# Optimization experiments

Measured on AMD Instinct MI355X. Metric: run time of the kernel, lower is better.

## Reference

```python
import jax, jax.numpy as jnp
import numpy as np

N = 100000
E = 1600000
DIMS = [128, 128, 64]


def _gcn_norm(edge_index, num_nodes):
    # PyG gcn_norm: add self-loops, symmetric normalization D^-1/2 (A+I) D^-1/2
    src, dst = edge_index[0], edge_index[1]
    loop = jnp.arange(num_nodes, dtype=src.dtype)
    src = jnp.concatenate([src, loop])
    dst = jnp.concatenate([dst, loop])
    deg = jax.ops.segment_sum(jnp.ones_like(src, dtype=jnp.float32), dst,
                              num_segments=num_nodes)
    dinv = jnp.where(deg > 0, jax.lax.rsqrt(deg), 0.0)
    w = dinv[src] * dinv[dst]  # [E+N]
    return src, dst, w


def _gcn_conv(x, src, dst, w, W, b):
    # transform first (cheaper when out_dim <= in_dim), then aggregate
    h = x @ W                                   # [N, out]
    msg = h[src] * w[:, None]                   # gather + scale  [E+N, out]
    out = jax.ops.segment_sum(msg, dst, num_segments=x.shape[0])
    return out + b


def setup_inputs() -> dict:
    key = jax.random.key(0)
    ks = jax.random.split(key, 6)
    x = jax.random.normal(ks[0], (N, DIMS[0]), dtype=jnp.float32)
    edge_index = jax.random.randint(ks[1], (2, E), 0, N, dtype=jnp.int64)
    # Glorot-style init for GCNConv weights, zero bias (PyG default)
    W1 = jax.random.normal(ks[2], (DIMS[0], DIMS[1]), dtype=jnp.float32) / np.sqrt(DIMS[0])
    b1 = jnp.zeros((DIMS[1],), dtype=jnp.float32)
    W2 = jax.random.normal(ks[3], (DIMS[1], DIMS[2]), dtype=jnp.float32) / np.sqrt(DIMS[1])
    b2 = jnp.zeros((DIMS[2],), dtype=jnp.float32)
    return {"x": x, "edge_index": edge_index, "W1": W1, "b1": b1, "W2": W2, "b2": b2}


def reference(x, edge_index, W1, b1, W2, b2):
    src, dst, w = _gcn_norm(edge_index, x.shape[0])
    h = _gcn_conv(x, src, dst, w, W1, b1)
    h = jax.nn.relu(h)
    # dropout is identity in eval mode (deterministic reference)
    out = _gcn_conv(h, src, dst, w, W2, b2)
    return out
```

## Files before the change

kernel.cpp:

```cpp
#include <hip/hip_runtime.h>
#include <hip/hip_fp16.h>

#define TPB 256
#define CHUNK 1024
#define EPB 4096
#define CSHIFT 8
#define AGG_BLOCKS 2048

typedef _Float16 half8 __attribute__((ext_vector_type(8)));
typedef float    f32x4 __attribute__((ext_vector_type(4)));


__global__ __launch_bounds__(256) void scanA_kernel(const int* __restrict__ cnt,
                                                    int* __restrict__ row_ptr,
                                                    int* __restrict__ chunk_sums, int n) {
    __shared__ int ls[256];
    const int t    = threadIdx.x;
    const int base = blockIdx.x * CHUNK;
    const int idx  = base + t * 4;
    int4 v = make_int4(0, 0, 0, 0);
    if (idx + 3 < n) v = *(const int4*)(cnt + idx);
    else {
        if (idx + 0 < n) v.x = cnt[idx + 0];
        if (idx + 1 < n) v.y = cnt[idx + 1];
        if (idx + 2 < n) v.z = cnt[idx + 2];
        if (idx + 3 < n) v.w = cnt[idx + 3];
    }
    int s0 = v.x, s1 = s0 + v.y, s2 = s1 + v.z, s3 = s2 + v.w;
    ls[t] = s3;
    __syncthreads();
    for (int off = 1; off < 256; off <<= 1) {
        int xv = (t >= off) ? ls[t - off] : 0;
        __syncthreads();
        ls[t] += xv;
        __syncthreads();
    }
    int excl = (t == 0) ? 0 : ls[t - 1];
    if (idx + 0 < n) row_ptr[idx + 0] = excl;
    if (idx + 1 < n) row_ptr[idx + 1] = excl + s0;
    if (idx + 2 < n) row_ptr[idx + 2] = excl + s1;
    if (idx + 3 < n) row_ptr[idx + 3] = excl + s2;
    if (t == 255) chunk_sums[blockIdx.x] = ls[255];
}

__global__ __launch_bounds__(256) void scanB_kernel(int* __restrict__ chunk_sums, int nch) {
    __shared__ int ls[256];
    const int t = threadIdx.x;
    ls[t] = (t < nch) ? chunk_sums[t] : 0;
    __syncthreads();
    for (int off = 1; off < 256; off <<= 1) {
        int xv = (t >= off) ? ls[t - off] : 0;
        __syncthreads();
        ls[t] += xv;
        __syncthreads();
    }
    if (t < nch) chunk_sums[t] = (t == 0) ? 0 : ls[t - 1];
}

__global__ __launch_bounds__(256) void scanC_kernel(int* __restrict__ row_ptr,
                                                    const int* __restrict__ chunk_sums, int n) {
    const int base = blockIdx.x * CHUNK;
    const int off  = chunk_sums[blockIdx.x];
    for (int k = threadIdx.x; k < CHUNK; k += 256) {
        int i = base + k;
        if (i < n) row_ptr[i] += off;
    }
}


__global__ __launch_bounds__(256) void hist_kernel(const int* __restrict__ dst,
                                                   int* __restrict__ hist_g,
                                                   int e, int nbc, int nblk) {
    __shared__ int hs[512];
    const int t = threadIdx.x;
    for (int i = t; i < nbc; i += 256) hs[i] = 0;
    __syncthreads();
    const int e0  = blockIdx.x * EPB;
    const int lim = min(e0 + EPB, e);
    for (int i = e0 + t; i < lim; i += 256)
        atomicAdd(&hs[dst[i] >> CSHIFT], 1);
    __syncthreads();
    for (int b = t; b < nbc; b += 256)
        hist_g[b * nblk + blockIdx.x] = hs[b];
}

__global__ __launch_bounds__(256) void partition_kernel(const int* __restrict__ src,
                                                        const int* __restrict__ dst,
                                                        const int* __restrict__ hist_scan,
                                                        int* __restrict__ pairs,
                                                        int e, int nbc, int nblk) {
    __shared__ int  hs[512];
    __shared__ int  lscan[512];
    __shared__ int  lfill[512];
    __shared__ int  base_s[512];
    __shared__ int  ls[256];
    __shared__ int2 sp[EPB];
    const int t = threadIdx.x;
    for (int i = t; i < nbc; i += 256) { hs[i] = 0; lfill[i] = 0; }
    __syncthreads();
    const int e0  = blockIdx.x * EPB;
    const int lim = min(e0 + EPB, e);
    for (int i = e0 + t; i < lim; i += 256)
        atomicAdd(&hs[dst[i] >> CSHIFT], 1);
    __syncthreads();
    int v0 = (2 * t     < nbc) ? hs[2 * t]     : 0;
    int v1 = (2 * t + 1 < nbc) ? hs[2 * t + 1] : 0;
    ls[t] = v0 + v1;
    __syncthreads();
    for (int off = 1; off < 256; off <<= 1) {
        int xv = (t >= off) ? ls[t - off] : 0;
        __syncthreads();
        ls[t] += xv;
        __syncthreads();
    }
    int excl = (t == 0) ? 0 : ls[t - 1];
    if (2 * t     < nbc) lscan[2 * t]     = excl;
    if (2 * t + 1 < nbc) lscan[2 * t + 1] = excl + v0;
    for (int b = t; b < nbc; b += 256) base_s[b] = hist_scan[b * nblk + blockIdx.x];
    __syncthreads();
    for (int i = e0 + t; i < lim; i += 256) {
        int d = dst[i];
        int b = d >> CSHIFT;
        int r = atomicAdd(&lfill[b], 1);
        sp[lscan[b] + r] = make_int2(src[i], d);
    }
    __syncthreads();
    const int cnt = lim - e0;
    for (int i = t; i < cnt; i += 256) {
        int2 pr = sp[i];
        int  b  = pr.y >> CSHIFT;
        pairs[base_s[b] + (i - lscan[b])] = pr.x | ((pr.y & 255) << 17);
    }
}

__global__ __launch_bounds__(256) void bucket_finalize_kernel(const int* __restrict__ pairs,
                                                              const int* __restrict__ hist_scan,
                                                              int* __restrict__ row_ptr,
                                                              float* __restrict__ dinv,
                                                              int* __restrict__ csr_src,
                                                              int n, int e, int nbc, int nblk) {
    __shared__ int cnt_s[256];
    __shared__ int fill[256];
    __shared__ int ls[256];
    const int b   = blockIdx.x;
    const int nb0 = b << CSHIFT;
    const int t   = threadIdx.x;
    const int r0  = hist_scan[b * nblk];
    const int r1  = (b + 1 < nbc) ? hist_scan[(b + 1) * nblk] : e;
    cnt_s[t] = 0;
    __syncthreads();
    for (int i = r0 + t; i < r1; i += 256)
        atomicAdd(&cnt_s[pairs[i] >> 17], 1);
    __syncthreads();
    int c = cnt_s[t];
    ls[t] = c;
    __syncthreads();
    for (int off = 1; off < 256; off <<= 1) {
        int xv = (t >= off) ? ls[t - off] : 0;
        __syncthreads();
        ls[t] += xv;
        __syncthreads();
    }
    int excl = (t == 0) ? 0 : ls[t - 1];
    int node = nb0 + t;
    if (node < n) {
        row_ptr[node] = r0 + excl;
        dinv[node]    = rsqrtf((float)(c + 1));
    }
    fill[t] = r0 + excl;
    __syncthreads();
    for (int i = r0 + t; i < r1; i += 256) {
        int pr = pairs[i];
        int p  = atomicAdd(&fill[pr >> 17], 1);
        csr_src[p] = pr & 0x1FFFF;
    }
    if (b == 0 && t == 0) row_ptr[n] = e;
}


template <int M, bool RELU, typename XT>
__global__ __launch_bounds__(256) void gemm_mfma_kernel(const XT* __restrict__ X,
                                                        const float* __restrict__ W,
                                                        const float* __restrict__ dinv,
                                                        __half* __restrict__ H, int nrows) {
    constexpr int NC = M / 16;
    __shared__ __align__(16) _Float16 Wf[NC * 4 * 64 * 8];

    const int tid = threadIdx.x;

    for (int f = tid; f < NC * 4 * 64; f += 256) {
        int c    = f >> 8;
        int i    = (f >> 6) & 3;
        int lane = f & 63;
        int quad = lane >> 4, n = lane & 15;
        const float* wp = W + (size_t)(i * 32 + quad * 8) * M + c * 16 + n;
        half8 hv;
#pragma unroll
        for (int j = 0; j < 8; ++j) hv[j] = (_Float16)wp[(size_t)j * M];
        ((half8*)Wf)[f] = hv;
    }
    __syncthreads();

    const int  wave = tid >> 6, lane = tid & 63;
    const int  quad = lane >> 4, n16 = lane & 15;
    const long rowbase = (long)blockIdx.x * 64 + wave * 16;

    long arow = rowbase + n16;
    const XT* xrow = X + (size_t)(arow < nrows ? arow : 0) * 128;
    half8 a[4];
    if constexpr (sizeof(XT) == 4) {
        const float4* xr = (const float4*)xrow;
#pragma unroll
        for (int i = 0; i < 4; ++i) {
            float4 x0 = xr[i * 8 + quad * 2];
            float4 x1 = xr[i * 8 + quad * 2 + 1];
            if (RELU) {
                x0.x = fmaxf(x0.x, 0.f); x0.y = fmaxf(x0.y, 0.f);
                x0.z = fmaxf(x0.z, 0.f); x0.w = fmaxf(x0.w, 0.f);
                x1.x = fmaxf(x1.x, 0.f); x1.y = fmaxf(x1.y, 0.f);
                x1.z = fmaxf(x1.z, 0.f); x1.w = fmaxf(x1.w, 0.f);
            }
            half8 hv;
            hv[0] = (_Float16)x0.x; hv[1] = (_Float16)x0.y;
            hv[2] = (_Float16)x0.z; hv[3] = (_Float16)x0.w;
            hv[4] = (_Float16)x1.x; hv[5] = (_Float16)x1.y;
            hv[6] = (_Float16)x1.z; hv[7] = (_Float16)x1.w;
            a[i] = hv;
        }
    } else {
        const half8* xr = (const half8*)xrow;
#pragma unroll
        for (int i = 0; i < 4; ++i) {
            half8 hv = xr[i * 4 + quad];
            if (RELU) {
#pragma unroll
                for (int j = 0; j < 8; ++j)
                    hv[j] = (hv[j] > (_Float16)0) ? hv[j] : (_Float16)0;
            }
            a[i] = hv;
        }
    }

    float dv[4];
#pragma unroll
    for (int r = 0; r < 4; ++r) {
        long orow = rowbase + quad * 4 + r;
        dv[r] = (orow < nrows) ? dinv[orow] : 0.f;
    }

    for (int c = 0; c < NC; ++c) {
        f32x4 acc = {0.f, 0.f, 0.f, 0.f};
#pragma unroll
        for (int i = 0; i < 4; ++i) {
            half8 b = ((const half8*)Wf)[(c * 4 + i) * 64 + lane];
            acc = __builtin_amdgcn_mfma_f32_16x16x32_f16(a[i], b, acc, 0, 0, 0);
        }
#pragma unroll
        for (int r = 0; r < 4; ++r) {
            long orow = rowbase + quad * 4 + r;
            if (orow < nrows)
                H[orow * M + c * 16 + n16] = __float2half(acc[r] * dv[r]);
        }
    }
}


__device__ __forceinline__ void add_u4(float2* a, const uint4& u) {
    float2 v0 = __half22float2(*(const __half2*)&u.x);
    float2 v1 = __half22float2(*(const __half2*)&u.y);
    float2 v2 = __half22float2(*(const __half2*)&u.z);
    float2 v3 = __half22float2(*(const __half2*)&u.w);
    a[0].x += v0.x; a[0].y += v0.y;
    a[1].x += v1.x; a[1].y += v1.y;
    a[2].x += v2.x; a[2].y += v2.y;
    a[3].x += v3.x; a[3].y += v3.y;
}


__global__ __launch_bounds__(TPB) void agg_pull128_kernel(const __half* __restrict__ hs,
                                                          const int* __restrict__ csr_src,
                                                          const int* __restrict__ row_ptr,
                                                          const float* __restrict__ dinv,
                                                          const float* __restrict__ bias,
                                                          __half* __restrict__ out, int n) {
    const int wid  = blockIdx.x * (TPB / 64) + (threadIdx.x >> 6);
    const int NW   = gridDim.x * (TPB / 64);
    const int lane = threadIdx.x & 63;
    const int q    = lane >> 4;
    const int sl   = lane & 15;
    if (wid >= n) return;
    const uint4* up   = (const uint4*)hs;
    const uint4* upsl = up + sl;

    const float4* bp = (const float4*)bias;
    const float4 bb0 = bp[2 * sl], bb1 = bp[2 * sl + 1];

    int b0 = row_ptr[wid], e0 = row_ptr[wid + 1];
    int nA = wid + NW;
    int b1 = 0, e1 = 0;
    if (nA < n) { b1 = row_ptr[nA]; e1 = row_ptr[nA + 1]; }
    int m0 = e0 - b0; if (m0 > 64) m0 = 64;
    int idx0 = (lane < m0) ? csr_src[b0 + lane] : 0;
    uint4 self0 = make_uint4(0, 0, 0, 0);
    if (q == 0) self0 = up[(size_t)wid * 16 + sl];
    float dv0 = dinv[wid];

    for (int ni = wid; ni < n; ni += NW) {
        const int n1 = ni + NW, n2 = ni + 2 * NW;
        int b2 = 0, e2 = 0;
        if (n2 < n) { b2 = row_ptr[n2]; e2 = row_ptr[n2 + 1]; }
        int idx1 = 0; uint4 self1 = make_uint4(0, 0, 0, 0); float dv1 = 0.f;
        if (n1 < n) {
            int m1 = e1 - b1; if (m1 > 64) m1 = 64;
            idx1 = (lane < m1) ? csr_src[b1 + lane] : 0;
            if (q == 0) self1 = up[(size_t)n1 * 16 + sl];
            dv1 = dinv[n1];
        }
        const int deg = e0 - b0;
        int m = deg; if (m > 64) m = 64;
        int sA0 = __shfl(idx0, q);
        int sA1 = __shfl(idx0, 4 + q);
        int sA2 = __shfl(idx0, 8 + q);
        int sA3 = __shfl(idx0, 12 + q);
        int sB0 = __shfl(idx0, 16 + q);
        int sB1 = __shfl(idx0, 20 + q);
        int sB2 = __shfl(idx0, 24 + q);
        int sB3 = __shfl(idx0, 28 + q);
        uint4 uA0 = upsl[(size_t)(unsigned)sA0 * 16];
        uint4 uA1 = upsl[(size_t)(unsigned)sA1 * 16];
        uint4 uA2 = upsl[(size_t)(unsigned)sA2 * 16];
        uint4 uA3 = upsl[(size_t)(unsigned)sA3 * 16];
        uint4 uB0 = upsl[(size_t)(unsigned)sB0 * 16];
        uint4 uB1 = upsl[(size_t)(unsigned)sB1 * 16];
        uint4 uB2 = upsl[(size_t)(unsigned)sB2 * 16];
        uint4 uB3 = upsl[(size_t)(unsigned)sB3 * 16];
        float2 a0[4], a1[4];
#pragma unroll
        for (int k = 0; k < 4; ++k) { a0[k] = make_float2(0.f, 0.f); a1[k] = make_float2(0.f, 0.f); }
        if (m >= 32) {
            add_u4(a0, uA0); add_u4(a1, uA1); add_u4(a0, uA2); add_u4(a1, uA3);
            add_u4(a0, uB0); add_u4(a1, uB1); add_u4(a0, uB2); add_u4(a1, uB3);
        } else {
            if (q < m)      add_u4(a0, uA0);
            if (4 + q < m)  add_u4(a1, uA1);
            if (8 + q < m)  add_u4(a0, uA2);
            if (12 + q < m) add_u4(a1, uA3);
            if (16 + q < m) add_u4(a0, uB0);
            if (20 + q < m) add_u4(a1, uB1);
            if (24 + q < m) add_u4(a0, uB2);
            if (28 + q < m) add_u4(a1, uB3);
        }
        for (int j = 32; j < m; j += 16) {
            int s0 = __shfl(idx0, j + q);
            int s1 = __shfl(idx0, j + 4 + q);
            int s2 = __shfl(idx0, j + 8 + q);
            int s3 = __shfl(idx0, j + 12 + q);
            uint4 u0 = upsl[(size_t)(unsigned)s0 * 16];
            uint4 u1 = upsl[(size_t)(unsigned)s1 * 16];
            uint4 u2 = upsl[(size_t)(unsigned)s2 * 16];
            uint4 u3 = upsl[(size_t)(unsigned)s3 * 16];
            if (j + q < m)      add_u4(a0, u0);
            if (j + 4 + q < m)  add_u4(a1, u1);
            if (j + 8 + q < m)  add_u4(a0, u2);
            if (j + 12 + q < m) add_u4(a1, u3);
        }
        for (int base = b0 + 64; base < e0; base += 64) {
            int mm = e0 - base; if (mm > 64) mm = 64;
            int idxv = (lane < mm) ? csr_src[base + lane] : 0;
            for (int j = 0; j < mm; j += 16) {
                int s0 = __shfl(idxv, j + q);
                int s1 = __shfl(idxv, j + 4 + q);
                int s2 = __shfl(idxv, j + 8 + q);
                int s3 = __shfl(idxv, j + 12 + q);
                uint4 u0 = upsl[(size_t)(unsigned)s0 * 16];
                uint4 u1 = upsl[(size_t)(unsigned)s1 * 16];
                uint4 u2 = upsl[(size_t)(unsigned)s2 * 16];
                uint4 u3 = upsl[(size_t)(unsigned)s3 * 16];
                if (j + q < mm)      add_u4(a0, u0);
                if (j + 4 + q < mm)  add_u4(a1, u1);
                if (j + 8 + q < mm)  add_u4(a0, u2);
                if (j + 12 + q < mm) add_u4(a1, u3);
            }
        }
#pragma unroll
        for (int k = 0; k < 4; ++k) { a0[k].x += a1[k].x; a0[k].y += a1[k].y; }
#pragma unroll
        for (int k = 0; k < 4; ++k) {
            a0[k].x += __shfl(a0[k].x, lane ^ 16);
            a0[k].y += __shfl(a0[k].y, lane ^ 16);
            a0[k].x += __shfl(a0[k].x, lane ^ 32);
            a0[k].y += __shfl(a0[k].y, lane ^ 32);
        }
        if (q == 0) {
            float2 v0 = __half22float2(*(const __half2*)&self0.x);
            float2 v1 = __half22float2(*(const __half2*)&self0.y);
            float2 v2 = __half22float2(*(const __half2*)&self0.z);
            float2 v3 = __half22float2(*(const __half2*)&self0.w);
            __half2 h0 = __floats2half2_rn(bb0.x + dv0 * (a0[0].x + v0.x),
                                           bb0.y + dv0 * (a0[0].y + v0.y));
            __half2 h1 = __floats2half2_rn(bb0.z + dv0 * (a0[1].x + v1.x),
                                           bb0.w + dv0 * (a0[1].y + v1.y));
            __half2 h2 = __floats2half2_rn(bb1.x + dv0 * (a0[2].x + v2.x),
                                           bb1.y + dv0 * (a0[2].y + v2.y));
            __half2 h3 = __floats2half2_rn(bb1.z + dv0 * (a0[3].x + v3.x),
                                           bb1.w + dv0 * (a0[3].y + v3.y));
            uint4 ov;
            ov.x = *(const unsigned*)&h0; ov.y = *(const unsigned*)&h1;
            ov.z = *(const unsigned*)&h2; ov.w = *(const unsigned*)&h3;
            ((uint4*)out)[(size_t)ni * 16 + sl] = ov;
        }
        b0 = b1; e0 = e1; idx0 = idx1; self0 = self1; dv0 = dv1;
        b1 = b2; e1 = e2;
    }
}


__global__ __launch_bounds__(TPB) void agg_pull64_kernel(const __half* __restrict__ hs,
                                                         const int* __restrict__ csr_src,
                                                         const int* __restrict__ row_ptr,
                                                         const float* __restrict__ dinv,
                                                         const float* __restrict__ bias,
                                                         float* __restrict__ out, int n) {
    const int wid  = blockIdx.x * (TPB / 64) + (threadIdx.x >> 6);
    const int NW   = gridDim.x * (TPB / 64);
    const int lane = threadIdx.x & 63;
    const int q    = lane >> 3;
    const int sl   = lane & 7;
    if (wid >= n) return;
    const uint4* up   = (const uint4*)hs;
    const uint4* upsl = up + sl;

    const float4* bp = (const float4*)bias;
    const float4 bb0 = bp[2 * sl], bb1 = bp[2 * sl + 1];

    int b0 = row_ptr[wid], e0 = row_ptr[wid + 1];
    int nA = wid + NW;
    int b1 = 0, e1 = 0;
    if (nA < n) { b1 = row_ptr[nA]; e1 = row_ptr[nA + 1]; }
    int m0 = e0 - b0; if (m0 > 64) m0 = 64;
    int idx0 = (lane < m0) ? csr_src[b0 + lane] : 0;
    uint4 self0 = make_uint4(0, 0, 0, 0);
    if (q == 0) self0 = up[(size_t)wid * 8 + sl];
    float dv0 = dinv[wid];

    for (int ni = wid; ni < n; ni += NW) {
        const int n1 = ni + NW, n2 = ni + 2 * NW;
        int b2 = 0, e2 = 0;
        if (n2 < n) { b2 = row_ptr[n2]; e2 = row_ptr[n2 + 1]; }
        int idx1 = 0; uint4 self1 = make_uint4(0, 0, 0, 0); float dv1 = 0.f;
        if (n1 < n) {
            int m1 = e1 - b1; if (m1 > 64) m1 = 64;
            idx1 = (lane < m1) ? csr_src[b1 + lane] : 0;
            if (q == 0) self1 = up[(size_t)n1 * 8 + sl];
            dv1 = dinv[n1];
        }
        const int deg = e0 - b0;
        int m = deg; if (m > 64) m = 64;
        int sA0 = __shfl(idx0, q);
        int sA1 = __shfl(idx0, 8 + q);
        int sB0 = __shfl(idx0, 16 + q);
        int sB1 = __shfl(idx0, 24 + q);
        uint4 uA0 = upsl[(size_t)(unsigned)sA0 * 8];
        uint4 uA1 = upsl[(size_t)(unsigned)sA1 * 8];
        uint4 uB0 = upsl[(size_t)(unsigned)sB0 * 8];
        uint4 uB1 = upsl[(size_t)(unsigned)sB1 * 8];
        float2 a0[4], a1[4];
#pragma unroll
        for (int k = 0; k < 4; ++k) { a0[k] = make_float2(0.f, 0.f); a1[k] = make_float2(0.f, 0.f); }
        if (m >= 32) {
            add_u4(a0, uA0); add_u4(a1, uA1); add_u4(a0, uB0); add_u4(a1, uB1);
        } else {
            if (q < m)      add_u4(a0, uA0);
            if (8 + q < m)  add_u4(a1, uA1);
            if (16 + q < m) add_u4(a0, uB0);
            if (24 + q < m) add_u4(a1, uB1);
        }
        for (int j = 32; j < m; j += 16) {
            int s0 = __shfl(idx0, j + q);
            int s1 = __shfl(idx0, j + 8 + q);
            uint4 u0 = upsl[(size_t)(unsigned)s0 * 8];
            uint4 u1 = upsl[(size_t)(unsigned)s1 * 8];
            if (j + q < m)     add_u4(a0, u0);
            if (j + 8 + q < m) add_u4(a1, u1);
        }
        for (int base = b0 + 64; base < e0; base += 64) {
            int mm = e0 - base; if (mm > 64) mm = 64;
            int idxv = (lane < mm) ? csr_src[base + lane] : 0;
            for (int j = 0; j < mm; j += 16) {
                int s0 = __shfl(idxv, j + q);
                int s1 = __shfl(idxv, j + 8 + q);
                uint4 u0 = upsl[(size_t)(unsigned)s0 * 8];
                uint4 u1 = upsl[(size_t)(unsigned)s1 * 8];
                if (j + q < mm)     add_u4(a0, u0);
                if (j + 8 + q < mm) add_u4(a1, u1);
            }
        }
#pragma unroll
        for (int k = 0; k < 4; ++k) { a0[k].x += a1[k].x; a0[k].y += a1[k].y; }
#pragma unroll
        for (int k = 0; k < 4; ++k) {
            a0[k].x += __shfl(a0[k].x, lane ^ 8);
            a0[k].y += __shfl(a0[k].y, lane ^ 8);
            a0[k].x += __shfl(a0[k].x, lane ^ 16);
            a0[k].y += __shfl(a0[k].y, lane ^ 16);
            a0[k].x += __shfl(a0[k].x, lane ^ 32);
            a0[k].y += __shfl(a0[k].y, lane ^ 32);
        }
        if (q == 0) {
            float2 v0 = __half22float2(*(const __half2*)&self0.x);
            float2 v1 = __half22float2(*(const __half2*)&self0.y);
            float2 v2 = __half22float2(*(const __half2*)&self0.z);
            float2 v3 = __half22float2(*(const __half2*)&self0.w);
            float4 o0, o1;
            o0.x = bb0.x + dv0 * (a0[0].x + v0.x);
            o0.y = bb0.y + dv0 * (a0[0].y + v0.y);
            o0.z = bb0.z + dv0 * (a0[1].x + v1.x);
            o0.w = bb0.w + dv0 * (a0[1].y + v1.y);
            o1.x = bb1.x + dv0 * (a0[2].x + v2.x);
            o1.y = bb1.y + dv0 * (a0[2].y + v2.y);
            o1.z = bb1.z + dv0 * (a0[3].x + v3.x);
            o1.w = bb1.w + dv0 * (a0[3].y + v3.y);
            ((float4*)out)[(size_t)ni * 16 + 2 * sl]     = o0;
            ((float4*)out)[(size_t)ni * 16 + 2 * sl + 1] = o1;
        }
        b0 = b1; e0 = e1; idx0 = idx1; self0 = self1; dv0 = dv1;
        b1 = b2; e1 = e2;
    }
}


extern "C" void kernel_launch(void* const* d_in, const int* in_sizes, int n_in,
                              void* d_out, int out_size, void* d_ws, size_t ws_size,
                              hipStream_t stream) {
    const float* x  = (const float*)d_in[0];
    const int*   ei = (const int*)d_in[1];
    const float* W1 = (const float*)d_in[2];
    const float* b1 = (const float*)d_in[3];
    const float* W2 = (const float*)d_in[4];
    const float* b2 = (const float*)d_in[5];
    float* out = (float*)d_out;

    const int N = in_sizes[0] / 128;
    const int E = in_sizes[1] / 2;
    const int* srcv = ei;
    const int* dstv = ei + E;

    const int NBC    = (N + 255) >> CSHIFT;
    const int NBLK_E = (E + EPB - 1) / EPB;
    const int HLEN   = NBC * NBLK_E;
    const int NCHH   = (HLEN + CHUNK - 1) / CHUNK;

    char* p = (char*)d_ws;
    int*    row_ptr    = (int*)p;    p += (((size_t)N + 64) * 4 + 63) & ~(size_t)63;
    int*    chunk_sums = (int*)p;    p += 1024;
    int*    hist       = (int*)p;    p += (((size_t)HLEN + 64) * 4 + 63) & ~(size_t)63;
    int*    csr_src    = (int*)p;    p += ((size_t)E * 4 + 63) & ~(size_t)63;
    float*  dinv       = (float*)p;  p += (((size_t)N + 64) * 4 + 63) & ~(size_t)63;
    __half* hs1        = (__half*)p; p += (size_t)N * 128 * 2;
    __half* out1       = (__half*)p; p += (size_t)N * 128 * 2;
    int*    pairs      = (int*)out1;
    __half* hs2        = hs1;

    hist_kernel<<<NBLK_E, 256, 0, stream>>>(dstv, hist, E, NBC, NBLK_E);
    scanA_kernel<<<NCHH, 256, 0, stream>>>(hist, hist, chunk_sums, HLEN);
    scanB_kernel<<<1, 256, 0, stream>>>(chunk_sums, NCHH);
    scanC_kernel<<<NCHH, 256, 0, stream>>>(hist, chunk_sums, HLEN);
    partition_kernel<<<NBLK_E, 256, 0, stream>>>(srcv, dstv, hist, pairs, E, NBC, NBLK_E);
    bucket_finalize_kernel<<<NBC, 256, 0, stream>>>(pairs, hist, row_ptr, dinv, csr_src,
                                                    N, E, NBC, NBLK_E);

    gemm_mfma_kernel<128, false, float><<<(N + 63) / 64, 256, 0, stream>>>(x, W1, dinv, hs1, N);
    agg_pull128_kernel<<<AGG_BLOCKS, TPB, 0, stream>>>(hs1, csr_src, row_ptr, dinv, b1, out1, N);

    gemm_mfma_kernel<64, true, _Float16><<<(N + 63) / 64, 256, 0, stream>>>(
        (const _Float16*)out1, W2, dinv, hs2, N);
    agg_pull64_kernel<<<AGG_BLOCKS, TPB, 0, stream>>>(hs2, csr_src, row_ptr, dinv, b2, out, N);
}
```

Baseline: 270.5 us.

## Fuse layer-2 GEMM into layer-1 aggregation and fold scan offsets into consumers

The layer-1 aggregation kernel now applies bias and ReLU, stages each node's 128-wide row in shared memory, and multiplies it by a shared-memory copy of W2. It writes the dinv-scaled 64-wide hs2 directly, which removes the separate second GEMM and the 128-wide fp16 intermediate round trip. The scanC kernel is dropped: partition and bucket_finalize add the chunk offsets themselves. Weight conversion to fp16 is hoisted into a small wprep kernel. In exchange, the per-node scalar FMA GEMV inside the aggregation loop adds ALU work and LDS traffic, and each block uses about 19KB of extra shared memory, which may reduce occupancy of this latency-bound gather kernel.

```diff
diff --git a/kernel.cpp b/kernel.cpp
--- a/kernel.cpp
+++ b/kernel.cpp
@@ -8,6 +8,7 @@
 #define AGG_BLOCKS 2048
 
 typedef _Float16 half8 __attribute__((ext_vector_type(8)));
+typedef _Float16 half4_t __attribute__((ext_vector_type(4)));
 typedef float    f32x4 __attribute__((ext_vector_type(4)));
 
 
@@ -57,16 +58,6 @@
     if (t < nch) chunk_sums[t] = (t == 0) ? 0 : ls[t - 1];
 }
 
-__global__ __launch_bounds__(256) void scanC_kernel(int* __restrict__ row_ptr,
-                                                    const int* __restrict__ chunk_sums, int n) {
-    const int base = blockIdx.x * CHUNK;
-    const int off  = chunk_sums[blockIdx.x];
-    for (int k = threadIdx.x; k < CHUNK; k += 256) {
-        int i = base + k;
-        if (i < n) row_ptr[i] += off;
-    }
-}
-
 
 __global__ __launch_bounds__(256) void hist_kernel(const int* __restrict__ dst,
                                                    int* __restrict__ hist_g,
@@ -87,6 +78,7 @@
 __global__ __launch_bounds__(256) void partition_kernel(const int* __restrict__ src,
                                                         const int* __restrict__ dst,
                                                         const int* __restrict__ hist_scan,
+                                                        const int* __restrict__ chunk_sums,
                                                         int* __restrict__ pairs,
                                                         int e, int nbc, int nblk) {
     __shared__ int  hs[512];
@@ -116,7 +108,10 @@
     int excl = (t == 0) ? 0 : ls[t - 1];
     if (2 * t     < nbc) lscan[2 * t]     = excl;
     if (2 * t + 1 < nbc) lscan[2 * t + 1] = excl + v0;
-    for (int b = t; b < nbc; b += 256) base_s[b] = hist_scan[b * nblk + blockIdx.x];
+    for (int b = t; b < nbc; b += 256) {
+        int hidx = b * nblk + blockIdx.x;
+        base_s[b] = hist_scan[hidx] + chunk_sums[hidx >> 10];
+    }
     __syncthreads();
     for (int i = e0 + t; i < lim; i += 256) {
         int d = dst[i];
@@ -135,6 +130,7 @@
 
 __global__ __launch_bounds__(256) void bucket_finalize_kernel(const int* __restrict__ pairs,
                                                               const int* __restrict__ hist_scan,
+                                                              const int* __restrict__ chunk_sums,
                                                               int* __restrict__ row_ptr,
                                                               float* __restrict__ dinv,
                                                               int* __restrict__ csr_src,
@@ -145,8 +141,13 @@
     const int b   = blockIdx.x;
     const int nb0 = b << CSHIFT;
     const int t   = threadIdx.x;
-    const int r0  = hist_scan[b * nblk];
-    const int r1  = (b + 1 < nbc) ? hist_scan[(b + 1) * nblk] : e;
+    const int h0  = b * nblk;
+    const int r0  = hist_scan[h0] + chunk_sums[h0 >> 10];
+    int r1 = e;
+    if (b + 1 < nbc) {
+        const int h1 = (b + 1) * nblk;
+        r1 = hist_scan[h1] + chunk_sums[h1 >> 10];
+    }
     cnt_s[t] = 0;
     __syncthreads();
     for (int i = r0 + t; i < r1; i += 256)
@@ -178,27 +179,45 @@
 }
 
 
-template <int M, bool RELU, typename XT>
-__global__ __launch_bounds__(256) void gemm_mfma_kernel(const XT* __restrict__ X,
-                                                        const float* __restrict__ W,
-                                                        const float* __restrict__ dinv,
-                                                        __half* __restrict__ H, int nrows) {
-    constexpr int NC = M / 16;
+__global__ __launch_bounds__(256) void wprep_kernel(const float* __restrict__ W1,
+                                                    const float* __restrict__ W2,
+                                                    _Float16* __restrict__ wf1g,
+                                                    _Float16* __restrict__ w2c) {
+    const int tid = threadIdx.x;
+    if (blockIdx.x == 0) {
+        for (int f = tid; f < 8 * 4 * 64; f += 256) {
+            int c    = f >> 8;
+            int i    = (f >> 6) & 3;
+            int lane = f & 63;
+            int quad = lane >> 4, n = lane & 15;
+            const float* wp = W1 + (size_t)(i * 32 + quad * 8) * 128 + c * 16 + n;
+            half8 hv;
+#pragma unroll
+            for (int j = 0; j < 8; ++j) hv[j] = (_Float16)wp[(size_t)j * 128];
+            ((half8*)wf1g)[f] = hv;
+        }
+    } else {
+        for (int idx = tid; idx < 64 * 128; idx += 256) {
+            int c = idx >> 7, k = idx & 127;
+            w2c[c * 132 + k] = (_Float16)W2[(size_t)k * 64 + c];
+        }
+        for (int idx = tid; idx < 64 * 4; idx += 256)
+            w2c[(idx >> 2) * 132 + 128 + (idx & 3)] = (_Float16)0.f;
+    }
+}
+
+
+__global__ __launch_bounds__(256) void gemm_mfma128_kernel(const float* __restrict__ X,
+                                                           const _Float16* __restrict__ Wfg,
+                                                           const float* __restrict__ dinv,
+                                                           __half* __restrict__ H, int nrows) {
+    constexpr int NC = 8;
     __shared__ __align__(16) _Float16 Wf[NC * 4 * 64 * 8];
 
     const int tid = threadIdx.x;
-
-    for (int f = tid; f < NC * 4 * 64; f += 256) {
-        int c    = f >> 8;
-        int i    = (f >> 6) & 3;
-        int lane = f & 63;
-        int quad = lane >> 4, n = lane & 15;
-        const float* wp = W + (size_t)(i * 32 + quad * 8) * M + c * 16 + n;
-        half8 hv;
-#pragma unroll
-        for (int j = 0; j < 8; ++j) hv[j] = (_Float16)wp[(size_t)j * M];
-        ((half8*)Wf)[f] = hv;
-    }
+    const uint4* wb = (const uint4*)Wfg;
+    for (int f = tid; f < NC * 4 * 64; f += 256)
+        ((uint4*)Wf)[f] = wb[f];
     __syncthreads();
 
     const int  wave = tid >> 6, lane = tid & 63;
@@ -206,39 +225,18 @@
     const long rowbase = (long)blockIdx.x * 64 + wave * 16;
 
     long arow = rowbase + n16;
-    const XT* xrow = X + (size_t)(arow < nrows ? arow : 0) * 128;
+    const float4* xr = (const float4*)(X + (size_t)(arow < nrows ? arow : 0) * 128);
     half8 a[4];
-    if constexpr (sizeof(XT) == 4) {
-        const float4* xr = (const float4*)xrow;
-#pragma unroll
-        for (int i = 0; i < 4; ++i) {
-            float4 x0 = xr[i * 8 + quad * 2];
-            float4 x1 = xr[i * 8 + quad * 2 + 1];
-            if (RELU) {
-                x0.x = fmaxf(x0.x, 0.f); x0.y = fmaxf(x0.y, 0.f);
-                x0.z = fmaxf(x0.z, 0.f); x0.w = fmaxf(x0.w, 0.f);
-                x1.x = fmaxf(x1.x, 0.f); x1.y = fmaxf(x1.y, 0.f);
-                x1.z = fmaxf(x1.z, 0.f); x1.w = fmaxf(x1.w, 0.f);
-            }
-            half8 hv;
-            hv[0] = (_Float16)x0.x; hv[1] = (_Float16)x0.y;
-            hv[2] = (_Float16)x0.z; hv[3] = (_Float16)x0.w;
-            hv[4] = (_Float16)x1.x; hv[5] = (_Float16)x1.y;
-            hv[6] = (_Float16)x1.z; hv[7] = (_Float16)x1.w;
-            a[i] = hv;
-        }
-    } else {
-        const half8* xr = (const half8*)xrow;
-#pragma unroll
-        for (int i = 0; i < 4; ++i) {
-            half8 hv = xr[i * 4 + quad];
-            if (RELU) {
-#pragma unroll
-                for (int j = 0; j < 8; ++j)
-                    hv[j] = (hv[j] > (_Float16)0) ? hv[j] : (_Float16)0;
-            }
-            a[i] = hv;
-        }
+#pragma unroll
+    for (int i = 0; i < 4; ++i) {
+        float4 x0 = xr[i * 8 + quad * 2];
+        float4 x1 = xr[i * 8 + quad * 2 + 1];
+        half8 hv;
+        hv[0] = (_Float16)x0.x; hv[1] = (_Float16)x0.y;
+        hv[2] = (_Float16)x0.z; hv[3] = (_Float16)x0.w;
+        hv[4] = (_Float16)x1.x; hv[5] = (_Float16)x1.y;
+        hv[6] = (_Float16)x1.z; hv[7] = (_Float16)x1.w;
+        a[i] = hv;
     }
 
     float dv[4];
@@ -259,7 +257,7 @@
         for (int r = 0; r < 4; ++r) {
             long orow = rowbase + quad * 4 + r;
             if (orow < nrows)
-                H[orow * M + c * 16 + n16] = __float2half(acc[r] * dv[r]);
+                H[orow * 128 + c * 16 + n16] = __float2half(acc[r] * dv[r]);
         }
     }
 }
@@ -277,20 +275,31 @@
 }
 
 
-__global__ __launch_bounds__(TPB) void agg_pull128_kernel(const __half* __restrict__ hs,
-                                                          const int* __restrict__ csr_src,
-                                                          const int* __restrict__ row_ptr,
-                                                          const float* __restrict__ dinv,
-                                                          const float* __restrict__ bias,
-                                                          __half* __restrict__ out, int n) {
-    const int wid  = blockIdx.x * (TPB / 64) + (threadIdx.x >> 6);
+__global__ __launch_bounds__(TPB) void agg_fused128_kernel(const __half* __restrict__ hs,
+                                                           const int* __restrict__ csr_src,
+                                                           const int* __restrict__ row_ptr,
+                                                           const float* __restrict__ dinv,
+                                                           const float* __restrict__ bias,
+                                                           const _Float16* __restrict__ w2c,
+                                                           __half* __restrict__ hs2, int n) {
+    __shared__ __align__(16) _Float16 w2l[64 * 132];
+    __shared__ __align__(16) float rowbuf[TPB / 64][128];
+
+    const int tid  = threadIdx.x;
+    for (int i = tid; i < 64 * 132 / 4; i += 256)
+        ((uint2*)w2l)[i] = ((const uint2*)w2c)[i];
+    __syncthreads();
+
+    const int wid  = blockIdx.x * (TPB / 64) + (tid >> 6);
     const int NW   = gridDim.x * (TPB / 64);
-    const int lane = threadIdx.x & 63;
+    const int wv   = tid >> 6;
+    const int lane = tid & 63;
     const int q    = lane >> 4;
     const int sl   = lane & 15;
     if (wid >= n) return;
     const uint4* up   = (const uint4*)hs;
     const uint4* upsl = up + sl;
+    const _Float16* wcol = w2l + lane * 132;
 
     const float4* bp = (const float4*)bias;
     const float4 bb0 = bp[2 * sl], bb1 = bp[2 * sl + 1];
@@ -316,8 +325,7 @@
             if (q == 0) self1 = up[(size_t)n1 * 16 + sl];
             dv1 = dinv[n1];
         }
-        const int deg = e0 - b0;
-        int m = deg; if (m > 64) m = 64;
+        int m = e0 - b0; if (m > 64) m = 64;
         int sA0 = __shfl(idx0, q);
         int sA1 = __shfl(idx0, 4 + q);
         int sA2 = __shfl(idx0, 8 + q);
@@ -396,18 +404,36 @@
             float2 v1 = __half22float2(*(const __half2*)&self0.y);
             float2 v2 = __half22float2(*(const __half2*)&self0.z);
             float2 v3 = __half22float2(*(const __half2*)&self0.w);
-            __half2 h0 = __floats2half2_rn(bb0.x + dv0 * (a0[0].x + v0.x),
-                                           bb0.y + dv0 * (a0[0].y + v0.y));
-            __half2 h1 = __floats2half2_rn(bb0.z + dv0 * (a0[1].x + v1.x),
-                                           bb0.w + dv0 * (a0[1].y + v1.y));
-            __half2 h2 = __floats2half2_rn(bb1.x + dv0 * (a0[2].x + v2.x),
-                                           bb1.y + dv0 * (a0[2].y + v2.y));
-            __half2 h3 = __floats2half2_rn(bb1.z + dv0 * (a0[3].x + v3.x),
-                                           bb1.w + dv0 * (a0[3].y + v3.y));
-            uint4 ov;
-            ov.x = *(const unsigned*)&h0; ov.y = *(const unsigned*)&h1;
-            ov.z = *(const unsigned*)&h2; ov.w = *(const unsigned*)&h3;
-            ((uint4*)out)[(size_t)ni * 16 + sl] = ov;
+            float4 w0, w1;
+            w0.x = fmaxf(bb0.x + dv0 * (a0[0].x + v0.x), 0.f);
+            w0.y = fmaxf(bb0.y + dv0 * (a0[0].y + v0.y), 0.f);
+            w0.z = fmaxf(bb0.z + dv0 * (a0[1].x + v1.x), 0.f);
+            w0.w = fmaxf(bb0.w + dv0 * (a0[1].y + v1.y), 0.f);
+            w1.x = fmaxf(bb1.x + dv0 * (a0[2].x + v2.x), 0.f);
+            w1.y = fmaxf(bb1.y + dv0 * (a0[2].y + v2.y), 0.f);
+            w1.z = fmaxf(bb1.z + dv0 * (a0[3].x + v3.x), 0.f);
+            w1.w = fmaxf(bb1.w + dv0 * (a0[3].y + v3.y), 0.f);
+            ((float4*)&rowbuf[wv][sl * 8])[0] = w0;
+            ((float4*)&rowbuf[wv][sl * 8])[1] = w1;
+        }
+        {
+            float acc[4] = {0.f, 0.f, 0.f, 0.f};
+#pragma unroll
+            for (int kc = 0; kc < 16; ++kc) {
+                const int k = kc * 8;
+                float4 r01 = *(const float4*)&rowbuf[wv][k];
+                float4 r23 = *(const float4*)&rowbuf[wv][k + 4];
+                half4_t wa = *(const half4_t*)&wcol[k];
+                half4_t wb2 = *(const half4_t*)&wcol[k + 4];
+                acc[kc & 3] += r01.x * (float)wa[0] + r01.y * (float)wa[1]
+                             + r01.z * (float)wa[2] + r01.w * (float)wa[3]
+                             + r23.x * (float)wb2[0] + r23.y * (float)wb2[1]
+                             + r23.z * (float)wb2[2] + r23.w * (float)wb2[3];
+            }
+            float val = dv0 * ((acc[0] + acc[1]) + (acc[2] + acc[3]));
+            float oth = __shfl(val, lane ^ 1);
+            if (!(lane & 1))
+                ((__half2*)hs2)[(size_t)ni * 32 + (lane >> 1)] = __floats2half2_rn(val, oth);
         }
         b0 = b1; e0 = e1; idx0 = idx1; self0 = self1; dv0 = dv1;
         b1 = b2; e1 = e2;
@@ -454,8 +480,7 @@
             if (q == 0) self1 = up[(size_t)n1 * 8 + sl];
             dv1 = dinv[n1];
         }
-        const int deg = e0 - b0;
-        int m = deg; if (m > 64) m = 64;
+        int m = e0 - b0; if (m > 64) m = 64;
         int sA0 = __shfl(idx0, q);
         int sA1 = __shfl(idx0, 8 + q);
         int sB0 = __shfl(idx0, 16 + q);
@@ -551,28 +576,31 @@
     const int NCHH   = (HLEN + CHUNK - 1) / CHUNK;
 
     char* p = (char*)d_ws;
-    int*    row_ptr    = (int*)p;    p += (((size_t)N + 64) * 4 + 63) & ~(size_t)63;
-    int*    chunk_sums = (int*)p;    p += 1024;
-    int*    hist       = (int*)p;    p += (((size_t)HLEN + 64) * 4 + 63) & ~(size_t)63;
-    int*    csr_src    = (int*)p;    p += ((size_t)E * 4 + 63) & ~(size_t)63;
-    float*  dinv       = (float*)p;  p += (((size_t)N + 64) * 4 + 63) & ~(size_t)63;
-    __half* hs1        = (__half*)p; p += (size_t)N * 128 * 2;
-    __half* out1       = (__half*)p; p += (size_t)N * 128 * 2;
-    int*    pairs      = (int*)out1;
-    __half* hs2        = hs1;
+    int*      row_ptr    = (int*)p;      p += (((size_t)N + 64) * 4 + 63) & ~(size_t)63;
+    int*      chunk_sums = (int*)p;      p += 1024;
+    int*      hist       = (int*)p;      p += (((size_t)HLEN + 64) * 4 + 63) & ~(size_t)63;
+    int*      csr_src    = (int*)p;      p += ((size_t)E * 4 + 63) & ~(size_t)63;
+    float*    dinv       = (float*)p;    p += (((size_t)N + 64) * 4 + 63) & ~(size_t)63;
+    _Float16* wf1g       = (_Float16*)p; p += 8 * 4 * 64 * 16;
+    _Float16* w2c        = (_Float16*)p; p += ((size_t)64 * 132 * 2 + 63) & ~(size_t)63;
+    __half*   hs1        = (__half*)p;   p += (size_t)N * 128 * 2;
+    __half*   hs2        = (__half*)p;   p += (size_t)N * 64 * 2;
+    int*      pairs      = (int*)hs2;
+
+    wprep_kernel<<<2, 256, 0, stream>>>(W1, W2, wf1g, w2c);
 
     hist_kernel<<<NBLK_E, 256, 0, stream>>>(dstv, hist, E, NBC, NBLK_E);
     scanA_kernel<<<NCHH, 256, 0, stream>>>(hist, hist, chunk_sums, HLEN);
     scanB_kernel<<<1, 256, 0, stream>>>(chunk_sums, NCHH);
-    scanC_kernel<<<NCHH, 256, 0, stream>>>(hist, chunk_sums, HLEN);
-    partition_kernel<<<NBLK_E, 256, 0, stream>>>(srcv, dstv, hist, pairs, E, NBC, NBLK_E);
-    bucket_finalize_kernel<<<NBC, 256, 0, stream>>>(pairs, hist, row_ptr, dinv, csr_src,
-                                                    N, E, NBC, NBLK_E);
-
-    gemm_mfma_kernel<128, false, float><<<(N + 63) / 64, 256, 0, stream>>>(x, W1, dinv, hs1, N);
-    agg_pull128_kernel<<<AGG_BLOCKS, TPB, 0, stream>>>(hs1, csr_src, row_ptr, dinv, b1, out1, N);
-
-    gemm_mfma_kernel<64, true, _Float16><<<(N + 63) / 64, 256, 0, stream>>>(
-        (const _Float16*)out1, W2, dinv, hs2, N);
+    partition_kernel<<<NBLK_E, 256, 0, stream>>>(srcv, dstv, hist, chunk_sums, pairs,
+                                                 E, NBC, NBLK_E);
+    bucket_finalize_kernel<<<NBC, 256, 0, stream>>>(pairs, hist, chunk_sums, row_ptr, dinv,
+                                                    csr_src, N, E, NBC, NBLK_E);
+
+    gemm_mfma128_kernel<<<(N + 63) / 64, 256, 0, stream>>>(x, wf1g, dinv, hs1, N);
+
+    agg_fused128_kernel<<<AGG_BLOCKS, TPB, 0, stream>>>(hs1, csr_src, row_ptr, dinv, b1,
+                                                        w2c, hs2, N);
+
     agg_pull64_kernel<<<AGG_BLOCKS, TPB, 0, stream>>>(hs2, csr_src, row_ptr, dinv, b2, out, N);
 }
```

After: 328.5 us. 21.5% more time.
